# Performance work log

Hardware: AMD Instinct MI355X
Metric: run time of the kernel (lower is better)

## Reference

```python
import jax, jax.numpy as jnp
import numpy as np

EPS = 1e-5


def _gcn_conv(x, src, dst, norm, W, b, n_nodes):
    # PyG GCNConv: transform, then normalized scatter-add aggregation (self-loops included in src/dst)
    h = x @ W                                   # [N, out]
    msg = h[src] * norm[:, None]                # gather over edges [E+N, out]
    agg = jax.ops.segment_sum(msg, dst, num_segments=n_nodes)
    return agg + b


def _bn(x, gamma, beta):
    # BatchNorm1d in training mode: batch stats over node axis, biased variance
    mu = jnp.mean(x, axis=0)
    var = jnp.mean((x - mu) ** 2, axis=0)
    return (x - mu) * jax.lax.rsqrt(var + EPS) * gamma + beta


def setup_inputs() -> dict:
    key = jax.random.key(0)
    ks = jax.random.split(key, 8)
    N, E, F_in, H, F_out = 50000, 800000, 32, 96, 2
    x = jax.random.normal(ks[0], (N, F_in), dtype=jnp.float32)
    edge_index = jax.random.randint(ks[1], (2, E), 0, N, dtype=jnp.int64)
    def lin(k, fi, fo):
        s = 1.0 / np.sqrt(fi)
        return jax.random.uniform(k, (fi, fo), jnp.float32, -s, s)
    W1 = lin(ks[2], F_in, H); b1 = jnp.zeros((H,), jnp.float32)
    W2 = lin(ks[3], H, H);    b2 = jnp.zeros((H,), jnp.float32)
    W3 = lin(ks[4], H, H);    b3 = jnp.zeros((H,), jnp.float32)
    W4 = lin(ks[5], H, F_out); b4 = jnp.zeros((F_out,), jnp.float32)
    g1 = jnp.ones((H,), jnp.float32); be1 = jnp.zeros((H,), jnp.float32)
    g2 = jnp.ones((H,), jnp.float32); be2 = jnp.zeros((H,), jnp.float32)
    g3 = jnp.ones((H,), jnp.float32); be3 = jnp.zeros((H,), jnp.float32)
    return dict(x=x, edge_index=edge_index,
                W1=W1, b1=b1, g1=g1, be1=be1,
                W2=W2, b2=b2, g2=g2, be2=be2,
                W3=W3, b3=b3, g3=g3, be3=be3,
                W4=W4, b4=b4)


def reference(x, edge_index, W1, b1, g1, be1, W2, b2, g2, be2, W3, b3, g3, be3, W4, b4):
    N = x.shape[0]
    loop = jnp.arange(N, dtype=edge_index.dtype)
    src = jnp.concatenate([edge_index[0], loop])   # add self-loops
    dst = jnp.concatenate([edge_index[1], loop])
    deg = jax.ops.segment_sum(jnp.ones_like(dst, dtype=x.dtype), dst, num_segments=N)
    dinv = jnp.where(deg > 0, jax.lax.rsqrt(deg), 0.0)
    norm = dinv[src] * dinv[dst]                   # D^{-1/2} (A+I) D^{-1/2}

    h = jax.nn.relu(_bn(_gcn_conv(x, src, dst, norm, W1, b1, N), g1, be1))
    h = jax.nn.relu(_bn(_gcn_conv(h, src, dst, norm, W2, b2, N), g2, be2))
    h = jax.nn.relu(_bn(_gcn_conv(h, src, dst, norm, W3, b3, N), g3, be3))
    return _gcn_conv(h, src, dst, norm, W4, b4, N)
```

## Files before the change

kernel.cpp:

```cpp
#include <hip/hip_runtime.h>
#include <hip/hip_bf16.h>

using bf16x8 = __attribute__((ext_vector_type(8))) short;
using f32x4  = __attribute__((ext_vector_type(4))) float;

#define FS_CHUNK 4096

__device__ __forceinline__ float ldf(const void* p, size_t i, float isf){
  if (isf > 0.5f) return ((const float*)p)[i];
  unsigned int u = ((unsigned int)((const unsigned short*)p)[i]) << 16;
  return __uint_as_float(u);
}
__device__ __forceinline__ unsigned short f2bf(float v){
  unsigned int u = __float_as_uint(v);
  u = (u + 0x7FFFu + ((u >> 16) & 1u)) >> 16;
  return (unsigned short)u;
}
__device__ __forceinline__ unsigned int pk2(float a, float b){
  return (unsigned int)f2bf(a) | ((unsigned int)f2bf(b) << 16);
}
__device__ __forceinline__ float lo16(unsigned int u){ return __uint_as_float(u << 16); }
__device__ __forceinline__ float hi16(unsigned int u){ return __uint_as_float(u & 0xFFFF0000u); }

__global__ void k_fill(unsigned short* o, unsigned short v, int n){
  int i = blockIdx.x*blockDim.x + threadIdx.x;
  if (i < n) o[i] = v;
}

__global__ void k_prep(const unsigned short* xh, const unsigned int* eu,
                       float* flag, int nelemX, long long E,
                       const void* W1, const void* W2, const void* W3, const void* W4,
                       unsigned short* __restrict__ Wt1, unsigned short* __restrict__ Wt2,
                       unsigned short* __restrict__ Wt3, float* __restrict__ W4f,
                       int* __restrict__ cnt, float* __restrict__ stAll, int n){
  int t = threadIdx.x;
  if (blockIdx.x > 0){
    int total = n + 4609;
    for (int i = (int)(blockIdx.x-1)*256 + t; i < total; i += (int)(gridDim.x-1)*256){
      if (i < n) cnt[i] = 0; else stAll[i - n] = 0.f;
    }
    return;
  }
  __shared__ int sf32, si64;
  __shared__ float sisf;
  if (t == 0){ sf32 = 0; si64 = 1; }
  __syncthreads();
  {
    int i = 2*t;
    if (i < nelemX){
      unsigned e8 = (xh[i] >> 7) & 0xFFu;
      if (e8 >= 140u) sf32 = 1;
    }
    if ((long long)(2*t + 1) < 2*E){
      if (eu[2*t + 1] != 0u) si64 = 0;
    }
  }
  __syncthreads();
  if (t == 0){
    flag[0] = (float)sf32; flag[1] = (float)si64;
    sisf = (float)sf32;
  }
  __syncthreads();
  float isf = sisf;
  for (int q = t; q < 3072; q += 256){
    int nn = q >> 5, k = q & 31;
    Wt1[q] = f2bf(ldf(W1, (size_t)96*k + nn, isf));
  }
  for (int q = t; q < 9216; q += 256){
    int nn = q/96, k = q - 96*nn;
    Wt2[q] = f2bf(ldf(W2, (size_t)96*k + nn, isf));
    Wt3[q] = f2bf(ldf(W3, (size_t)96*k + nn, isf));
  }
  if (t < 192) W4f[t] = ldf(W4, t, isf);
}

__global__ void k_cnt(const int* __restrict__ ei, const float* __restrict__ flag,
                      int* __restrict__ cnt, long long E, int n){
  long long i = (long long)blockIdx.x*blockDim.x + threadIdx.x;
  if (i >= E) return;
  int d = (flag[1] > 0.5f) ? ei[2*E + 2*i] : ei[E + i];
  if ((unsigned)d < (unsigned)n) atomicAdd(&cnt[d], 1);
}

__global__ void k_emit2(const int* __restrict__ cnt, int* __restrict__ gctr,
                        int* __restrict__ rowst, int* __restrict__ cursor,
                        float* __restrict__ dinv, int n){
  int i = blockIdx.x*256 + threadIdx.x;
  int lane = threadIdx.x & 63;
  int v = (i < n) ? cnt[i] : 0;
  int s = v;
  #pragma unroll
  for (int off = 1; off < 64; off <<= 1){
    int u = __shfl_up(s, off, 64);
    if (lane >= off) s += u;
  }
  int wtot = __shfl(s, 63, 64);
  int base = 0;
  if (lane == 63) base = atomicAdd(gctr, wtot);
  base = __shfl(base, 63, 64);
  if (i < n){
    int r = base + s - v;
    rowst[i]  = r;
    cursor[i] = r;
    dinv[i]   = rsqrtf((float)(1 + v));
  }
}

template<typename IT>
__global__ __launch_bounds__(256) void k_fl1(const int* __restrict__ ei,
      const float* __restrict__ flag, int* __restrict__ cursor, IT* __restrict__ csr,
      long long E, int n, int gF8,
      const void* __restrict__ x, const unsigned short* __restrict__ Wt1b,
      const float* __restrict__ dinv, unsigned short* __restrict__ HS){
  __shared__ __align__(16) unsigned short Xs[64][40];
  __shared__ __align__(16) unsigned short Wt[96][40];
  int t = threadIdx.x;
  if ((int)blockIdx.x < gF8){
    int part = blockIdx.x & 7;
    long long base = (long long)(blockIdx.x >> 3) * FS_CHUNK;
    int pl = (int)(((long long)n *  part     ) >> 3);
    int pr = (int)(((long long)n * (part + 1)) >> 3);
    bool i64 = (flag[1] > 0.5f);
    long long lim = base + FS_CHUNK < E ? base + FS_CHUNK : E;
    for (long long i = base + t; i < lim; i += 256){
      int s, d;
      if (i64){ s = ei[2*i]; d = ei[2*E + 2*i]; }
      else    { s = ei[i];   d = ei[E + i];     }
      if (d >= pl && d < pr && (unsigned)s < (unsigned)n){
        int p = atomicAdd(&cursor[d], 1);
        csr[p] = (IT)s;
      }
    }
    return;
  }
  int bid = blockIdx.x - gF8;
  float isf = flag[0];
  for (int q = t; q < 384; q += 256){
    uint4 v = ((const uint4*)Wt1b)[q];
    *(uint4*)&Wt[q >> 2][(q & 3)*8] = v;
  }
  {
    int row = t >> 2, part = t & 3;
    int node = bid*64 + row;
    uint4 o;
    if (node < n){
      if (isf > 0.5f){
        const float* xr = (const float*)x + (size_t)32*node + 8*part;
        o.x = pk2(xr[0], xr[1]); o.y = pk2(xr[2], xr[3]);
        o.z = pk2(xr[4], xr[5]); o.w = pk2(xr[6], xr[7]);
      } else {
        o = ((const uint4*)x)[(size_t)4*node + part];
      }
    } else { o.x = o.y = o.z = o.w = 0u; }
    *(uint4*)&Xs[row][8*part] = o;
  }
  __syncthreads();
  int wv = t >> 6, lane = t & 63;
  int m = lane & 15, quad = lane >> 4;
  bf16x8 av = *(const bf16x8*)&Xs[16*wv + m][8*quad];
  f32x4 acc[6];
  #pragma unroll
  for (int c = 0; c < 6; ++c) acc[c] = (f32x4)(0.f);
  #pragma unroll
  for (int c = 0; c < 6; ++c){
    bf16x8 bv = *(const bf16x8*)&Wt[16*c + m][8*quad];
    acc[c] = __builtin_amdgcn_mfma_f32_16x16x32_bf16(av, bv, acc[c], 0, 0, 0);
  }
  int rowbase = bid*64 + 16*wv + 4*quad;
  float div[4];
  #pragma unroll
  for (int r = 0; r < 4; ++r){ int rr = rowbase + r; div[r] = (rr < n) ? dinv[rr] : 0.f; }
  #pragma unroll
  for (int c = 0; c < 6; ++c){
    int col = 16*c + m;
    #pragma unroll
    for (int r = 0; r < 4; ++r){
      int rr = rowbase + r;
      if (rr < n) HS[(size_t)96*rr + col] = f2bf(acc[c][r]*div[r]);
    }
  }
}

#define ACC8(v) { a0+=lo16((v).x); a1+=hi16((v).x); a2+=lo16((v).y); a3+=hi16((v).y); \
                  a4+=lo16((v).z); a5+=hi16((v).z); a6+=lo16((v).w); a7+=hi16((v).w); }
template<typename IT>
__global__ __launch_bounds__(192) void k_agg(const uint4* __restrict__ hsr,
      const int* __restrict__ rowst, const int* __restrict__ cnt,
      const IT* __restrict__ csr,
      const float* __restrict__ dinv, uint4* __restrict__ zb4,
      float* __restrict__ stout, int n){
  __shared__ float ls[16][97], lq[16][97];
  int g = threadIdx.x, ty = threadIdx.y;
  int t = ty*12 + g;
  int node = blockIdx.x*16 + ty;
  float r[8];
  if (node < n){
    uint4 v = hsr[(size_t)node*12 + g];
    float a0 = lo16(v.x), a1 = hi16(v.x), a2 = lo16(v.y), a3 = hi16(v.y);
    float a4 = lo16(v.z), a5 = hi16(v.z), a6 = lo16(v.w), a7 = hi16(v.w);
    int b = rowst[node], e = b + cnt[node];
    int j = b;
    for (; j + 7 < e; j += 8){
      uint4 v0 = hsr[(size_t)csr[j]  *12 + g];
      uint4 v1 = hsr[(size_t)csr[j+1]*12 + g];
      uint4 v2 = hsr[(size_t)csr[j+2]*12 + g];
      uint4 v3 = hsr[(size_t)csr[j+3]*12 + g];
      uint4 v4 = hsr[(size_t)csr[j+4]*12 + g];
      uint4 v5 = hsr[(size_t)csr[j+5]*12 + g];
      uint4 v6 = hsr[(size_t)csr[j+6]*12 + g];
      uint4 v7 = hsr[(size_t)csr[j+7]*12 + g];
      ACC8(v0); ACC8(v1); ACC8(v2); ACC8(v3);
      ACC8(v4); ACC8(v5); ACC8(v6); ACC8(v7);
    }
    for (; j + 3 < e; j += 4){
      uint4 v0 = hsr[(size_t)csr[j]  *12 + g];
      uint4 v1 = hsr[(size_t)csr[j+1]*12 + g];
      uint4 v2 = hsr[(size_t)csr[j+2]*12 + g];
      uint4 v3 = hsr[(size_t)csr[j+3]*12 + g];
      ACC8(v0); ACC8(v1); ACC8(v2); ACC8(v3);
    }
    for (; j < e; ++j){
      uint4 vv = hsr[(size_t)csr[j]*12 + g];
      ACC8(vv);
    }
    float di = dinv[node];
    uint4 o;
    o.x = pk2(a0*di, a1*di);
    o.y = pk2(a2*di, a3*di);
    o.z = pk2(a4*di, a5*di);
    o.w = pk2(a6*di, a7*di);
    zb4[(size_t)node*12 + g] = o;
    r[0]=lo16(o.x); r[1]=hi16(o.x); r[2]=lo16(o.y); r[3]=hi16(o.y);
    r[4]=lo16(o.z); r[5]=hi16(o.z); r[6]=lo16(o.w); r[7]=hi16(o.w);
  } else {
    #pragma unroll
    for (int jj = 0; jj < 8; ++jj) r[jj] = 0.f;
  }
  #pragma unroll
  for (int jj = 0; jj < 8; ++jj){
    ls[ty][8*g + jj] = r[jj];
    lq[ty][8*g + jj] = r[jj]*r[jj];
  }
  __syncthreads();
  if (t < 96){
    float s = 0.f, q = 0.f;
    #pragma unroll
    for (int rr = 0; rr < 16; ++rr){ s += ls[rr][t]; q += lq[rr][t]; }
    int rep = blockIdx.x & 7;
    atomicAdd(&stout[192*rep + t],      s);
    atomicAdd(&stout[192*rep + 96 + t], q);
  }
}

__global__ __launch_bounds__(256) void k_linm(const unsigned short* __restrict__ zb,
      const unsigned short* __restrict__ Wtb, const float* __restrict__ st,
      const void* __restrict__ gam, const void* __restrict__ bet,
      const float* __restrict__ flag, const float* __restrict__ dinv,
      unsigned short* __restrict__ HS, int n, float invN){
  __shared__ float sa[96], sc[96];
  __shared__ __align__(16) unsigned short Ys[64][104];
  __shared__ __align__(16) unsigned short Wt[96][104];
  int t = threadIdx.x;
  if (t < 96){
    float ssum = 0.f, qsum = 0.f;
    #pragma unroll
    for (int r = 0; r < 8; ++r){ ssum += st[192*r + t]; qsum += st[192*r + 96 + t]; }
    float isf = flag[0];
    float mu  = ssum*invN;
    float var = fmaxf(qsum*invN - mu*mu, 0.f);
    float istd = rsqrtf(var + 1e-5f);
    float a = ldf(gam, t, isf)*istd;
    sa[t] = a; sc[t] = ldf(bet, t, isf) - mu*a;
  }
  for (int q = t; q < 1152; q += 256){
    uint4 v = ((const uint4*)Wtb)[q];
    *(uint4*)&Wt[q/12][8*(q - 12*(q/12))] = v;
  }
  __syncthreads();
  {
    int row = t >> 2, part = t & 3;
    int node = blockIdx.x*64 + row;
    if (node < n){
      const uint4* zr = (const uint4*)(zb + (size_t)96*node) + 3*part;
      #pragma unroll
      for (int q = 0; q < 3; ++q){
        uint4 zz = zr[q];
        int k = 24*part + 8*q;
        float y0 = fmaxf(lo16(zz.x)*sa[k]   + sc[k],   0.f);
        float y1 = fmaxf(hi16(zz.x)*sa[k+1] + sc[k+1], 0.f);
        float y2 = fmaxf(lo16(zz.y)*sa[k+2] + sc[k+2], 0.f);
        float y3 = fmaxf(hi16(zz.y)*sa[k+3] + sc[k+3], 0.f);
        float y4 = fmaxf(lo16(zz.z)*sa[k+4] + sc[k+4], 0.f);
        float y5 = fmaxf(hi16(zz.z)*sa[k+5] + sc[k+5], 0.f);
        float y6 = fmaxf(lo16(zz.w)*sa[k+6] + sc[k+6], 0.f);
        float y7 = fmaxf(hi16(zz.w)*sa[k+7] + sc[k+7], 0.f);
        *(unsigned int*)&Ys[row][k]     = pk2(y0, y1);
        *(unsigned int*)&Ys[row][k + 2] = pk2(y2, y3);
        *(unsigned int*)&Ys[row][k + 4] = pk2(y4, y5);
        *(unsigned int*)&Ys[row][k + 6] = pk2(y6, y7);
      }
    } else {
      unsigned int* yp = (unsigned int*)&Ys[row][24*part];
      #pragma unroll
      for (int q = 0; q < 12; ++q) yp[q] = 0u;
    }
  }
  __syncthreads();
  int wv = t >> 6, lane = t & 63;
  int m = lane & 15, quad = lane >> 4;
  bf16x8 av[3];
  #pragma unroll
  for (int kt = 0; kt < 3; ++kt)
    av[kt] = *(const bf16x8*)&Ys[16*wv + m][32*kt + 8*quad];
  f32x4 acc[6];
  #pragma unroll
  for (int c = 0; c < 6; ++c) acc[c] = (f32x4)(0.f);
  #pragma unroll
  for (int c = 0; c < 6; ++c){
    const unsigned short* wrow = &Wt[16*c + m][8*quad];
    #pragma unroll
    for (int kt = 0; kt < 3; ++kt){
      bf16x8 bv = *(const bf16x8*)(wrow + 32*kt);
      acc[c] = __builtin_amdgcn_mfma_f32_16x16x32_bf16(av[kt], bv, acc[c], 0, 0, 0);
    }
  }
  int rowbase = blockIdx.x*64 + 16*wv + 4*quad;
  float div[4];
  #pragma unroll
  for (int r = 0; r < 4; ++r){ int rr = rowbase + r; div[r] = (rr < n) ? dinv[rr] : 0.f; }
  #pragma unroll
  for (int c = 0; c < 6; ++c){
    int col = 16*c + m;
    #pragma unroll
    for (int r = 0; r < 4; ++r){
      int rr = rowbase + r;
      if (rr < n) HS[(size_t)96*rr + col] = f2bf(acc[c][r]*div[r]);
    }
  }
}

__global__ __launch_bounds__(256) void k_lin4(const unsigned short* __restrict__ zb,
      const float* __restrict__ Wf, const float* __restrict__ st,
      const void* __restrict__ gam, const void* __restrict__ bet,
      const float* __restrict__ flag, const float* __restrict__ dinv,
      float* __restrict__ hs2, int n, float invN){
  __shared__ float sa[96], sc[96];
  int t = threadIdx.x;
  if (t < 96){
    float ssum = 0.f, qsum = 0.f;
    #pragma unroll
    for (int r = 0; r < 8; ++r){ ssum += st[192*r + t]; qsum += st[192*r + 96 + t]; }
    float isf = flag[0];
    float mu  = ssum*invN;
    float var = fmaxf(qsum*invN - mu*mu, 0.f);
    float istd = rsqrtf(var + 1e-5f);
    float a = ldf(gam, t, isf)*istd;
    sa[t] = a; sc[t] = ldf(bet, t, isf) - mu*a;
  }
  __syncthreads();
  int i = blockIdx.x*blockDim.x + t;
  if (i >= n) return;
  const uint4* zr = (const uint4*)(zb + (size_t)96*i);
  float a0 = 0.f, a1 = 0.f;
  #pragma unroll
  for (int q = 0; q < 12; ++q){
    uint4 zz = zr[q];
    int k = 8*q;
    float y;
    y = fmaxf(lo16(zz.x)*sa[k]   + sc[k],   0.f); a0 += y*Wf[2*k];    a1 += y*Wf[2*k+1];
    y = fmaxf(hi16(zz.x)*sa[k+1] + sc[k+1], 0.f); a0 += y*Wf[2*k+2];  a1 += y*Wf[2*k+3];
    y = fmaxf(lo16(zz.y)*sa[k+2] + sc[k+2], 0.f); a0 += y*Wf[2*k+4];  a1 += y*Wf[2*k+5];
    y = fmaxf(hi16(zz.y)*sa[k+3] + sc[k+3], 0.f); a0 += y*Wf[2*k+6];  a1 += y*Wf[2*k+7];
    y = fmaxf(lo16(zz.z)*sa[k+4] + sc[k+4], 0.f); a0 += y*Wf[2*k+8];  a1 += y*Wf[2*k+9];
    y = fmaxf(hi16(zz.z)*sa[k+5] + sc[k+5], 0.f); a0 += y*Wf[2*k+10]; a1 += y*Wf[2*k+11];
    y = fmaxf(lo16(zz.w)*sa[k+6] + sc[k+6], 0.f); a0 += y*Wf[2*k+12]; a1 += y*Wf[2*k+13];
    y = fmaxf(hi16(zz.w)*sa[k+7] + sc[k+7], 0.f); a0 += y*Wf[2*k+14]; a1 += y*Wf[2*k+15];
  }
  float di = dinv[i];
  hs2[(size_t)2*i]   = di*a0;
  hs2[(size_t)2*i+1] = di*a1;
}

template<typename IT>
__global__ void k_agg2(const float2* __restrict__ hs2, const int* __restrict__ rowst,
                       const int* __restrict__ cnt, const IT* __restrict__ csr,
                       const float* __restrict__ dinv,
                       const void* __restrict__ b4, const float* __restrict__ flag,
                       void* __restrict__ out, int n){
  int node = blockIdx.x*blockDim.x + threadIdx.x;
  if (node >= n) return;
  float2 a = hs2[node];
  int b = rowst[node], e = b + cnt[node];
  int j = b;
  for (; j + 3 < e; j += 4){
    float2 v0 = hs2[(size_t)csr[j]];
    float2 v1 = hs2[(size_t)csr[j+1]];
    float2 v2 = hs2[(size_t)csr[j+2]];
    float2 v3 = hs2[(size_t)csr[j+3]];
    a.x += v0.x + v1.x + v2.x + v3.x;
    a.y += v0.y + v1.y + v2.y + v3.y;
  }
  for (; j < e; ++j){
    float2 v = hs2[(size_t)csr[j]];
    a.x += v.x; a.y += v.y;
  }
  float isf = flag[0];
  float di = dinv[node];
  float v0 = a.x*di + ldf(b4, 0, isf);
  float v1 = a.y*di + ldf(b4, 1, isf);
  if (isf > 0.5f){
    ((float*)out)[(size_t)2*node]   = v0;
    ((float*)out)[(size_t)2*node+1] = v1;
  } else {
    ((unsigned short*)out)[(size_t)2*node]   = f2bf(v0);
    ((unsigned short*)out)[(size_t)2*node+1] = f2bf(v1);
  }
}

extern "C" void kernel_launch(void* const* d_in, const int* in_sizes, int n_in,
                              void* d_out, int out_size, void* d_ws, size_t ws_size,
                              hipStream_t stream)
{
  const int B = 256;
  unsigned short* outh = (unsigned short*)d_out;

  if (n_in < 16){
    k_fill<<<(out_size+B-1)/B, B, 0, stream>>>(outh, 0x3F40u, out_size); return;
  }
  const int N = in_sizes[0] / 32;
  const long long E = in_sizes[1] / 2;
  if (in_sizes[0] % 32 != 0 || out_size != 2*N){
    k_fill<<<(out_size+B-1)/B, B, 0, stream>>>(outh, 0x3F60u, out_size); return;
  }
  const bool u16 = (N < 65536);

  size_t Npad = ((size_t)N + 3) & ~(size_t)3;
  float* ws   = (float*)d_ws;
  float* dinv = ws;
  float* hs2  = dinv + Npad;
  float* flag = hs2 + (size_t)2*N;
  float* stAll= flag + 4;
  float* W4f  = stAll + 4612;
  unsigned short* Wt1b = (unsigned short*)(W4f + 192);
  unsigned short* Wt2b = Wt1b + 3072;
  unsigned short* Wt3b = Wt2b + 9216;
  int* cnt    = (int*)(Wt3b + 9216);
  int* cursor = cnt + N;
  int* rowst  = cursor + N;
  void* csrv  = (void*)(rowst + N);
  size_t csrBytes = (size_t)E * (u16 ? 2 : 4);
  uintptr_t hp_ = (uintptr_t)csrv + csrBytes;
  hp_ = (hp_ + 15) & ~(uintptr_t)15;
  unsigned short* HS = (unsigned short*)hp_;
  unsigned short* Zb = HS + (size_t)96*N;

  size_t needB = ((uintptr_t)(Zb + (size_t)96*N) - (uintptr_t)d_ws) + 64;
  if (ws_size < needB){
    k_fill<<<(out_size+B-1)/B, B, 0, stream>>>(outh, 0x3F00u, out_size); return;
  }

  const void* x  = d_in[0];
  const int*  ei = (const int*)d_in[1];
  const void* W1 = d_in[2];
  const void* g1 = d_in[4];  const void* be1 = d_in[5];
  const void* W2 = d_in[6];
  const void* g2 = d_in[8];  const void* be2 = d_in[9];
  const void* W3 = d_in[10];
  const void* g3 = d_in[12]; const void* be3 = d_in[13];
  const void* W4 = d_in[14];
  const void* b4 = d_in[15];

  float* stA = stAll;
  float* stB = stAll + 1536;
  float* stC = stAll + 3072;
  int*   gctr = (int*)(stAll + 4608);

  int gN  = (N + B - 1)/B;
  int gE  = (int)((E + B - 1)/B);
  int nb  = (N + 255)/256;
  int gA  = (N + 15)/16;
  int gL  = (N + 63)/64;
  int gF8 = (int)((E + FS_CHUNK - 1)/FS_CHUNK) * 8;
  float invN = 1.0f / (float)N;
  dim3 ablk(12,16);

  k_prep<<<33, B, 0, stream>>>((const unsigned short*)x, (const unsigned int*)ei,
                               flag, in_sizes[0], E, W1, W2, W3, W4,
                               Wt1b, Wt2b, Wt3b, W4f, cnt, stAll, N);
  k_cnt<<<gE, B, 0, stream>>>(ei, flag, cnt, E, N);
  k_emit2<<<nb, B, 0, stream>>>(cnt, gctr, rowst, cursor, dinv, N);

  if (u16){
    unsigned short* csr = (unsigned short*)csrv;
    k_fl1<unsigned short><<<gF8 + gL, B, 0, stream>>>(ei, flag, cursor, csr, E, N, gF8,
                                                      x, Wt1b, dinv, HS);
    k_agg<unsigned short><<<gA, ablk, 0, stream>>>((const uint4*)HS, rowst, cnt, csr, dinv, (uint4*)Zb, stA, N);
    k_linm<<<gL, B, 0, stream>>>(Zb, Wt2b, stA, g1, be1, flag, dinv, HS, N, invN);
    k_agg<unsigned short><<<gA, ablk, 0, stream>>>((const uint4*)HS, rowst, cnt, csr, dinv, (uint4*)Zb, stB, N);
    k_linm<<<gL, B, 0, stream>>>(Zb, Wt3b, stB, g2, be2, flag, dinv, HS, N, invN);
    k_agg<unsigned short><<<gA, ablk, 0, stream>>>((const uint4*)HS, rowst, cnt, csr, dinv, (uint4*)Zb, stC, N);
    k_lin4<<<gN, B, 0, stream>>>(Zb, W4f, stC, g3, be3, flag, dinv, hs2, N, invN);
    k_agg2<unsigned short><<<gN, B, 0, stream>>>((const float2*)hs2, rowst, cnt, csr, dinv, b4, flag, d_out, N);
  } else {
    int* csr = (int*)csrv;
    k_fl1<int><<<gF8 + gL, B, 0, stream>>>(ei, flag, cursor, csr, E, N, gF8,
                                           x, Wt1b, dinv, HS);
    k_agg<int><<<gA, ablk, 0, stream>>>((const uint4*)HS, rowst, cnt, csr, dinv, (uint4*)Zb, stA, N);
    k_linm<<<gL, B, 0, stream>>>(Zb, Wt2b, stA, g1, be1, flag, dinv, HS, N, invN);
    k_agg<int><<<gA, ablk, 0, stream>>>((const uint4*)HS, rowst, cnt, csr, dinv, (uint4*)Zb, stB, N);
    k_linm<<<gL, B, 0, stream>>>(Zb, Wt3b, stB, g2, be2, flag, dinv, HS, N, invN);
    k_agg<int><<<gA, ablk, 0, stream>>>((const uint4*)HS, rowst, cnt, csr, dinv, (uint4*)Zb, stC, N);
    k_lin4<<<gN, B, 0, stream>>>(Zb, W4f, stC, g3, be3, flag, dinv, hs2, N, invN);
    k_agg2<int><<<gN, B, 0, stream>>>((const float2*)hs2, rowst, cnt, csr, dinv, b4, flag, d_out, N);
  }
}
```

Baseline: 338.7 us.

## Aggregate raw 32-wide features before layer-1 transform and compact edge list

Layer 1 now aggregates the dinv-scaled 32-channel input features over the CSR first, then applies W1 with MFMA in the same kernel and accumulates BN stats. Gathers therefore read 32-wide rows instead of 96-wide transformed rows. Separately, the count kernel writes a packed, validated (src,dst) int array so the CSR fill reads it with vector loads instead of re-reading the possibly int64 edge_index. This adds an extra E*8-byte workspace buffer and changes the rounding order of layer 1 (aggregate then bf16 matmul).

Measured after the change: 329.9 us. 2.6% less time.

```diff
diff --git a/kernel.cpp b/kernel.cpp
--- a/kernel.cpp
+++ b/kernel.cpp
@@ -74,12 +74,44 @@
   if (t < 192) W4f[t] = ldf(W4, t, isf);
 }
 
-__global__ void k_cnt(const int* __restrict__ ei, const float* __restrict__ flag,
-                      int* __restrict__ cnt, long long E, int n){
+__global__ void k_cnt2(const int* __restrict__ ei, const float* __restrict__ flag,
+                       int* __restrict__ cnt, int* __restrict__ ec,
+                       long long E, int n){
   long long i = (long long)blockIdx.x*blockDim.x + threadIdx.x;
-  if (i >= E) return;
-  int d = (flag[1] > 0.5f) ? ei[2*E + 2*i] : ei[E + i];
-  if ((unsigned)d < (unsigned)n) atomicAdd(&cnt[d], 1);
+  long long i0 = 2*i;
+  if (i0 >= E) return;
+  bool i64 = (flag[1] > 0.5f);
+  bool two = (i0 + 1 < E);
+  int s0, d0, s1 = 0, d1 = -1;
+  if ((E & 1LL) == 0){
+    if (i64){
+      uint4 vs = ((const uint4*)ei)[i];
+      uint4 vd = ((const uint4*)(ei + 2*E))[i];
+      s0 = (int)vs.x; s1 = (int)vs.z; d0 = (int)vd.x; d1 = (int)vd.z;
+    } else {
+      int2 vs = ((const int2*)ei)[i];
+      int2 vd = ((const int2*)(ei + E))[i];
+      s0 = vs.x; s1 = vs.y; d0 = vd.x; d1 = vd.y;
+    }
+  } else {
+    if (i64){ s0 = ei[2*i0]; d0 = ei[2*E + 2*i0];
+              if (two){ s1 = ei[2*i0+2]; d1 = ei[2*E + 2*i0 + 2]; } }
+    else    { s0 = ei[i0];   d0 = ei[E + i0];
+              if (two){ s1 = ei[i0+1];   d1 = ei[E + i0 + 1]; } }
+  }
+  bool ok0 = ((unsigned)s0 < (unsigned)n) && ((unsigned)d0 < (unsigned)n);
+  bool ok1 = two && ((unsigned)s1 < (unsigned)n) && ((unsigned)d1 < (unsigned)n);
+  if (!ok0){ s0 = -1; d0 = -1; }
+  if (!ok1){ s1 = -1; d1 = -1; }
+  if (two){
+    int4 o; o.x = s0; o.y = d0; o.z = s1; o.w = d1;
+    ((int4*)ec)[i] = o;
+  } else {
+    int2 o; o.x = s0; o.y = d0;
+    ((int2*)ec)[i0] = o;
+  }
+  if (ok0) atomicAdd(&cnt[d0], 1);
+  if (ok1) atomicAdd(&cnt[d1], 1);
 }
 
 __global__ void k_emit2(const int* __restrict__ cnt, int* __restrict__ gctr,
@@ -107,53 +139,107 @@
 }
 
 template<typename IT>
-__global__ __launch_bounds__(256) void k_fl1(const int* __restrict__ ei,
-      const float* __restrict__ flag, int* __restrict__ cursor, IT* __restrict__ csr,
+__global__ __launch_bounds__(256) void k_fx(const int* __restrict__ ec,
+      int* __restrict__ cursor, IT* __restrict__ csr,
       long long E, int n, int gF8,
-      const void* __restrict__ x, const unsigned short* __restrict__ Wt1b,
-      const float* __restrict__ dinv, unsigned short* __restrict__ HS){
-  __shared__ __align__(16) unsigned short Xs[64][40];
-  __shared__ __align__(16) unsigned short Wt[96][40];
+      const void* __restrict__ x, const float* __restrict__ flag,
+      const float* __restrict__ dinv, unsigned short* __restrict__ XS){
   int t = threadIdx.x;
   if ((int)blockIdx.x < gF8){
     int part = blockIdx.x & 7;
     long long base = (long long)(blockIdx.x >> 3) * FS_CHUNK;
     int pl = (int)(((long long)n *  part     ) >> 3);
     int pr = (int)(((long long)n * (part + 1)) >> 3);
-    bool i64 = (flag[1] > 0.5f);
     long long lim = base + FS_CHUNK < E ? base + FS_CHUNK : E;
-    for (long long i = base + t; i < lim; i += 256){
-      int s, d;
-      if (i64){ s = ei[2*i]; d = ei[2*E + 2*i]; }
-      else    { s = ei[i];   d = ei[E + i];     }
-      if (d >= pl && d < pr && (unsigned)s < (unsigned)n){
-        int p = atomicAdd(&cursor[d], 1);
-        csr[p] = (IT)s;
+    for (long long i = base + 2*t; i < lim; i += 512){
+      int4 v = ((const int4*)ec)[i >> 1];
+      if (v.y >= pl && v.y < pr && (unsigned)v.x < (unsigned)n){
+        int p = atomicAdd(&cursor[v.y], 1);
+        csr[p] = (IT)v.x;
       }
+      if (i + 1 < lim && v.w >= pl && v.w < pr && (unsigned)v.z < (unsigned)n){
+        int p = atomicAdd(&cursor[v.w], 1);
+        csr[p] = (IT)v.z;
+      }
     }
     return;
   }
-  int bid = blockIdx.x - gF8;
-  float isf = flag[0];
+  int q = (int)(blockIdx.x - gF8)*256 + t;
+  if (q < 4*n){
+    int node = q >> 2, part = q & 3;
+    float isf = flag[0];
+    float di = dinv[node];
+    uint4 o;
+    if (isf > 0.5f){
+      const float* xr = (const float*)x + (size_t)32*node + 8*part;
+      o.x = pk2(xr[0]*di, xr[1]*di); o.y = pk2(xr[2]*di, xr[3]*di);
+      o.z = pk2(xr[4]*di, xr[5]*di); o.w = pk2(xr[6]*di, xr[7]*di);
+    } else {
+      uint4 v = ((const uint4*)x)[(size_t)4*node + part];
+      o.x = pk2(lo16(v.x)*di, hi16(v.x)*di);
+      o.y = pk2(lo16(v.y)*di, hi16(v.y)*di);
+      o.z = pk2(lo16(v.z)*di, hi16(v.z)*di);
+      o.w = pk2(lo16(v.w)*di, hi16(v.w)*di);
+    }
+    ((uint4*)XS)[q] = o;
+  }
+}
+
+#define ACC8(v) { a0+=lo16((v).x); a1+=hi16((v).x); a2+=lo16((v).y); a3+=hi16((v).y); \
+                  a4+=lo16((v).z); a5+=hi16((v).z); a6+=lo16((v).w); a7+=hi16((v).w); }
+
+template<typename IT>
+__global__ __launch_bounds__(256) void k_aggx(const uint4* __restrict__ xs4,
+      const int* __restrict__ rowst, const int* __restrict__ cnt,
+      const IT* __restrict__ csr, const float* __restrict__ dinv,
+      const unsigned short* __restrict__ Wt1b,
+      unsigned short* __restrict__ Zb, float* __restrict__ stout, int n){
+  __shared__ __align__(16) unsigned short Xs[64][40];
+  __shared__ __align__(16) unsigned short Wt[96][40];
+  __shared__ float bs[96], bq[96];
+  int t = threadIdx.x;
   for (int q = t; q < 384; q += 256){
     uint4 v = ((const uint4*)Wt1b)[q];
     *(uint4*)&Wt[q >> 2][(q & 3)*8] = v;
   }
-  {
-    int row = t >> 2, part = t & 3;
-    int node = bid*64 + row;
-    uint4 o;
-    if (node < n){
-      if (isf > 0.5f){
-        const float* xr = (const float*)x + (size_t)32*node + 8*part;
-        o.x = pk2(xr[0], xr[1]); o.y = pk2(xr[2], xr[3]);
-        o.z = pk2(xr[4], xr[5]); o.w = pk2(xr[6], xr[7]);
-      } else {
-        o = ((const uint4*)x)[(size_t)4*node + part];
-      }
-    } else { o.x = o.y = o.z = o.w = 0u; }
-    *(uint4*)&Xs[row][8*part] = o;
-  }
+  if (t < 96){ bs[t] = 0.f; bq[t] = 0.f; }
+  int g = t & 3, ty = t >> 2;
+  int node = blockIdx.x*64 + ty;
+  float a0=0.f,a1=0.f,a2=0.f,a3=0.f,a4=0.f,a5=0.f,a6=0.f,a7=0.f;
+  if (node < n){
+    uint4 v = xs4[(size_t)node*4 + g];
+    ACC8(v);
+    int b = rowst[node], e = b + cnt[node];
+    int j = b;
+    for (; j + 7 < e; j += 8){
+      uint4 v0 = xs4[(size_t)csr[j]  *4 + g];
+      uint4 v1 = xs4[(size_t)csr[j+1]*4 + g];
+      uint4 v2 = xs4[(size_t)csr[j+2]*4 + g];
+      uint4 v3 = xs4[(size_t)csr[j+3]*4 + g];
+      uint4 v4 = xs4[(size_t)csr[j+4]*4 + g];
+      uint4 v5 = xs4[(size_t)csr[j+5]*4 + g];
+      uint4 v6 = xs4[(size_t)csr[j+6]*4 + g];
+      uint4 v7 = xs4[(size_t)csr[j+7]*4 + g];
+      ACC8(v0); ACC8(v1); ACC8(v2); ACC8(v3);
+      ACC8(v4); ACC8(v5); ACC8(v6); ACC8(v7);
+    }
+    for (; j + 3 < e; j += 4){
+      uint4 v0 = xs4[(size_t)csr[j]  *4 + g];
+      uint4 v1 = xs4[(size_t)csr[j+1]*4 + g];
+      uint4 v2 = xs4[(size_t)csr[j+2]*4 + g];
+      uint4 v3 = xs4[(size_t)csr[j+3]*4 + g];
+      ACC8(v0); ACC8(v1); ACC8(v2); ACC8(v3);
+    }
+    for (; j < e; ++j){
+      uint4 vv = xs4[(size_t)csr[j]*4 + g];
+      ACC8(vv);
+    }
+    float di = dinv[node];
+    a0*=di; a1*=di; a2*=di; a3*=di; a4*=di; a5*=di; a6*=di; a7*=di;
+  }
+  uint4 o;
+  o.x = pk2(a0,a1); o.y = pk2(a2,a3); o.z = pk2(a4,a5); o.w = pk2(a6,a7);
+  *(uint4*)&Xs[ty][8*g] = o;
   __syncthreads();
   int wv = t >> 6, lane = t & 63;
   int m = lane & 15, quad = lane >> 4;
@@ -166,23 +252,32 @@
     bf16x8 bv = *(const bf16x8*)&Wt[16*c + m][8*quad];
     acc[c] = __builtin_amdgcn_mfma_f32_16x16x32_bf16(av, bv, acc[c], 0, 0, 0);
   }
-  int rowbase = bid*64 + 16*wv + 4*quad;
-  float div[4];
-  #pragma unroll
-  for (int r = 0; r < 4; ++r){ int rr = rowbase + r; div[r] = (rr < n) ? dinv[rr] : 0.f; }
+  int rowbase = blockIdx.x*64 + 16*wv + 4*quad;
   #pragma unroll
   for (int c = 0; c < 6; ++c){
     int col = 16*c + m;
+    float s = 0.f, q = 0.f;
     #pragma unroll
     for (int r = 0; r < 4; ++r){
       int rr = rowbase + r;
-      if (rr < n) HS[(size_t)96*rr + col] = f2bf(acc[c][r]*div[r]);
-    }
-  }
-}
-
-#define ACC8(v) { a0+=lo16((v).x); a1+=hi16((v).x); a2+=lo16((v).y); a3+=hi16((v).y); \
-                  a4+=lo16((v).z); a5+=hi16((v).z); a6+=lo16((v).w); a7+=hi16((v).w); }
+      if (rr < n){
+        unsigned short h = f2bf(acc[c][r]);
+        Zb[(size_t)96*rr + col] = h;
+        float br = __uint_as_float(((unsigned int)h) << 16);
+        s += br; q += br*br;
+      }
+    }
+    atomicAdd(&bs[col], s);
+    atomicAdd(&bq[col], q);
+  }
+  __syncthreads();
+  if (t < 96){
+    int rep = blockIdx.x & 7;
+    atomicAdd(&stout[192*rep + t],      bs[t]);
+    atomicAdd(&stout[192*rep + 96 + t], bq[t]);
+  }
+}
+
 template<typename IT>
 __global__ __launch_bounds__(192) void k_agg(const uint4* __restrict__ hsr,
       const int* __restrict__ rowst, const int* __restrict__ cnt,
@@ -453,11 +548,14 @@
   hp_ = (hp_ + 15) & ~(uintptr_t)15;
   unsigned short* HS = (unsigned short*)hp_;
   unsigned short* Zb = HS + (size_t)96*N;
-
-  size_t needB = ((uintptr_t)(Zb + (size_t)96*N) - (uintptr_t)d_ws) + 64;
+  int* ec = (int*)(Zb + (size_t)96*N);
+
+  size_t needB = ((uintptr_t)(ec + 2*E + 4) - (uintptr_t)d_ws) + 64;
   if (ws_size < needB){
     k_fill<<<(out_size+B-1)/B, B, 0, stream>>>(outh, 0x3F00u, out_size); return;
   }
+
+  unsigned short* XS = HS;
 
   const void* x  = d_in[0];
   const int*  ei = (const int*)d_in[1];
@@ -476,10 +574,12 @@
   int*   gctr = (int*)(stAll + 4608);
 
   int gN  = (N + B - 1)/B;
-  int gE  = (int)((E + B - 1)/B);
+  long long hE = (E + 1)/2;
+  int gE2 = (int)((hE + B - 1)/B); if (gE2 < 1) gE2 = 1;
   int nb  = (N + 255)/256;
   int gA  = (N + 15)/16;
   int gL  = (N + 63)/64;
+  int gXS = (4*N + 255)/256;
   int gF8 = (int)((E + FS_CHUNK - 1)/FS_CHUNK) * 8;
   float invN = 1.0f / (float)N;
   dim3 ablk(12,16);
@@ -487,14 +587,14 @@
   k_prep<<<33, B, 0, stream>>>((const unsigned short*)x, (const unsigned int*)ei,
                                flag, in_sizes[0], E, W1, W2, W3, W4,
                                Wt1b, Wt2b, Wt3b, W4f, cnt, stAll, N);
-  k_cnt<<<gE, B, 0, stream>>>(ei, flag, cnt, E, N);
+  k_cnt2<<<gE2, B, 0, stream>>>(ei, flag, cnt, ec, E, N);
   k_emit2<<<nb, B, 0, stream>>>(cnt, gctr, rowst, cursor, dinv, N);
 
   if (u16){
     unsigned short* csr = (unsigned short*)csrv;
-    k_fl1<unsigned short><<<gF8 + gL, B, 0, stream>>>(ei, flag, cursor, csr, E, N, gF8,
-                                                      x, Wt1b, dinv, HS);
-    k_agg<unsigned short><<<gA, ablk, 0, stream>>>((const uint4*)HS, rowst, cnt, csr, dinv, (uint4*)Zb, stA, N);
+    k_fx<unsigned short><<<gF8 + gXS, B, 0, stream>>>(ec, cursor, csr, E, N, gF8,
+                                                      x, flag, dinv, XS);
+    k_aggx<unsigned short><<<gL, B, 0, stream>>>((const uint4*)XS, rowst, cnt, csr, dinv, Wt1b, Zb, stA, N);
     k_linm<<<gL, B, 0, stream>>>(Zb, Wt2b, stA, g1, be1, flag, dinv, HS, N, invN);
     k_agg<unsigned short><<<gA, ablk, 0, stream>>>((const uint4*)HS, rowst, cnt, csr, dinv, (uint4*)Zb, stB, N);
     k_linm<<<gL, B, 0, stream>>>(Zb, Wt3b, stB, g2, be2, flag, dinv, HS, N, invN);
@@ -503,9 +603,9 @@
     k_agg2<unsigned short><<<gN, B, 0, stream>>>((const float2*)hs2, rowst, cnt, csr, dinv, b4, flag, d_out, N);
   } else {
     int* csr = (int*)csrv;
-    k_fl1<int><<<gF8 + gL, B, 0, stream>>>(ei, flag, cursor, csr, E, N, gF8,
-                                           x, Wt1b, dinv, HS);
-    k_agg<int><<<gA, ablk, 0, stream>>>((const uint4*)HS, rowst, cnt, csr, dinv, (uint4*)Zb, stA, N);
+    k_fx<int><<<gF8 + gXS, B, 0, stream>>>(ec, cursor, csr, E, N, gF8,
+                                           x, flag, dinv, XS);
+    k_aggx<int><<<gL, B, 0, stream>>>((const uint4*)XS, rowst, cnt, csr, dinv, Wt1b, Zb, stA, N);
     k_linm<<<gL, B, 0, stream>>>(Zb, Wt2b, stA, g1, be1, flag, dinv, HS, N, invN);
     k_agg<int><<<gA, ablk, 0, stream>>>((const uint4*)HS, rowst, cnt, csr, dinv, (uint4*)Zb, stB, N);
     k_linm<<<gL, B, 0, stream>>>(Zb, Wt3b, stB, g2, be2, flag, dinv, HS, N, invN);
```
